# Performance work log

Measured on AMD Instinct MI355X. Metric: run time of the kernel, lower is better.

The kernel has to match this reference:

```python
import jax, jax.numpy as jnp
import numpy as np

B, T, D, H = 512, 256, 128, 512


def setup_inputs() -> dict:
    key = jax.random.key(0)
    ks = jax.random.split(key, 12)
    stdv_g = 1.0 / np.sqrt(D)            # gate layers: in_features = 2D + H
    gin = 2 * D + H
    stdv_gate = 1.0 / np.sqrt(gin)
    u = lambda k, shape, s: jax.random.uniform(k, shape, jnp.float32, -s, s)
    inp = {
        "x": jax.random.normal(ks[0], (B, T, D), jnp.float32),
        "x_last_obsv": jax.random.normal(ks[1], (B, T, D), jnp.float32),
        "mask": (jax.random.uniform(ks[2], (B, T, D)) < 0.7).astype(jnp.float32),
        "delta": jax.random.uniform(ks[3], (B, T, D)) * 5.0,
        "x_mean": jnp.zeros((1, 1, D), jnp.float32),
        "Wz": u(ks[4], (H, gin), stdv_gate), "bz": u(ks[5], (H,), stdv_gate),
        "Wr": u(ks[6], (H, gin), stdv_gate), "br": u(ks[7], (H,), stdv_gate),
        "Wn": u(ks[8], (H, gin), stdv_gate), "bn": u(ks[9], (H,), stdv_gate),
        "Wgx": u(ks[10], (D, D), stdv_g), "bgx": u(ks[11], (D,), stdv_g),
        "Wgh": u(jax.random.fold_in(key, 100), (H, D), stdv_g),
        "bgh": u(jax.random.fold_in(key, 101), (H,), stdv_g),
    }
    return inp


def reference(x, x_last_obsv, mask, delta, x_mean, Wz, bz, Wr, br, Wn, bn,
              Wgx, bgx, Wgh, bgh):
    D_ = x.shape[-1]
    xbar = x_mean.reshape(-1)                      # (D,)
    Wgx_diag = jnp.eye(D_, dtype=Wgx.dtype) * Wgx  # FilterLinear diagonal mask

    def step(h, inputs):
        xt, xl, mt, dt = inputs                    # each (B, D)
        # input decay (Eq. 3): gamma_x = exp(-relu(W_gx @ delta + b))
        gx = jnp.exp(-jnp.maximum(0.0, dt @ Wgx_diag.T + bgx))
        x_tilde = mt * xt + (1.0 - mt) * (gx * xl + (1.0 - gx) * xbar)
        # hidden decay: gamma_h = exp(-relu(W_gh @ delta + b))
        gh = jnp.exp(-jnp.maximum(0.0, dt @ Wgh.T + bgh))
        h = gh * h
        comb = jnp.concatenate([x_tilde, h, mt], axis=1)   # (B, 2D+H)
        z = jax.nn.sigmoid(comb @ Wz.T + bz)
        r = jax.nn.sigmoid(comb @ Wr.T + br)
        comb_r = jnp.concatenate([x_tilde, r * h, mt], axis=1)
        h_tilde = jnp.tanh(comb_r @ Wn.T + bn)
        h = (1.0 - z) * h + z * h_tilde
        return h, None

    h0 = jnp.zeros((x.shape[0], Wz.shape[0]), x.dtype)
    seq = (jnp.swapaxes(x, 0, 1), jnp.swapaxes(x_last_obsv, 0, 1),
           jnp.swapaxes(mask, 0, 1), jnp.swapaxes(delta, 0, 1))  # (T, B, D)
    h_final, _ = jax.lax.scan(step, h0, seq)
    return h_final
```

## Files before the change

### kernel.cpp

```cpp
#include <hip/hip_runtime.h>
#include <hip/hip_bf16.h>
#include <cstdint>

typedef short v8s __attribute__((ext_vector_type(8)));
typedef float f32x4 __attribute__((ext_vector_type(4)));
typedef float f4 __attribute__((ext_vector_type(4)));

#define BB 512
#define TT 256
#define DD 128
#define HH 512
#define GINW 768

static __device__ __forceinline__ unsigned short f2b(float f) {
  __hip_bfloat16 h = __float2bfloat16(f);
  return __builtin_bit_cast(unsigned short, h);
}
static __device__ __forceinline__ unsigned long long pk4(float a, float b, float c, float d) {
  return (unsigned long long)f2b(a) | ((unsigned long long)f2b(b) << 16)
       | ((unsigned long long)f2b(c) << 32) | ((unsigned long long)f2b(d) << 48);
}
static __device__ __forceinline__ float sigm(float v) { return 1.f / (1.f + __expf(-v)); }
static __device__ __forceinline__ float tanh_f(float v) { return 1.f - 2.f / (__expf(2.f * v) + 1.f); }

#define MFMA(A, B, C) __builtin_amdgcn_mfma_f32_16x16x32_bf16((A), (B), (C), 0, 0, 0)

static __device__ __forceinline__ void load_frags16T(const unsigned short* base, v8s fr[16]) {
#pragma unroll
  for (int ks = 0; ks < 16; ++ks) {
    asm volatile("global_load_dwordx4 %0, %1, off sc0 sc1"
                 : "=v"(fr[ks]) : "v"(base + ks * 1024));
  }
  asm volatile("s_waitcnt vmcnt(0)" ::: "memory");
  __builtin_amdgcn_sched_barrier(0);
}

__global__ __launch_bounds__(256, 1) void k_seq(
    const float* __restrict__ x, const float* __restrict__ xl,
    const float* __restrict__ mk, const float* __restrict__ de,
    const float* __restrict__ xmean,
    const float* __restrict__ Wz, const float* __restrict__ bz,
    const float* __restrict__ Wr, const float* __restrict__ br,
    const float* __restrict__ Wn, const float* __restrict__ bn,
    const float* __restrict__ Wgx, const float* __restrict__ bgx,
    const float* __restrict__ Wgh, const float* __restrict__ bgh,
    unsigned short* __restrict__ PBUF, unsigned short* __restrict__ HBUF,
    unsigned int* __restrict__ BAR, float* __restrict__ out)
{
  __shared__ unsigned short XA[2][32 * 264];
  __shared__ unsigned short DLs[2][32 * 136];
  __shared__ unsigned short sl[32 * 36];
  __shared__ float cw[128], cbx[128], cxm[128];

  const int bid = blockIdx.x;
  const int g = bid & 15, j = bid >> 4;
  const int tid = threadIdx.x, wave = tid >> 6, lane = tid & 63;
  const int q = lane >> 4, ln = lane & 15;
  const int mh = wave >> 1, nh = wave & 1;
  const int b0 = g * 32, c0 = j * 32;
  const int mrow = mh * 16 + q * 4;
  const int arow = mh * 16 + ln;
  const int ccol = c0 + nh * 16 + ln;

  if (tid < 128) { cw[tid] = Wgx[tid * DD + tid]; cbx[tid] = bgx[tid]; cxm[tid] = xmean[tid]; }

  const float bzv = bz[ccol], brv = br[ccol], bnv = bn[ccol], bgv = bgh[ccol];

  v8s zb[16], rb[16], nb[16];
  {
    const size_t wro = (size_t)ccol * GINW + 128;
#pragma unroll
    for (int ks = 0; ks < 16; ++ks) {
      const float* pz = Wz + wro + ks * 32 + q * 8;
      const float* pr = Wr + wro + ks * 32 + q * 8;
      const float* pn = Wn + wro + ks * 32 + q * 8;
      v8s vz, vr, vn;
#pragma unroll
      for (int e = 0; e < 8; ++e) {
        vz[e] = (short)f2b(pz[e]); vr[e] = (short)f2b(pr[e]); vn[e] = (short)f2b(pn[e]);
      }
      zb[ks] = vz; rb[ks] = vr; nb[ks] = vn;
    }
  }
  v8s xzb[8], xrb[8], xnb[8];
  {
    const size_t wro = (size_t)ccol * GINW;
#pragma unroll
    for (int ks = 0; ks < 8; ++ks) {
      const size_t o = wro + ((ks < 4) ? (size_t)(ks * 32 + q * 8) : (size_t)(512 + ks * 32 + q * 8));
      const float* pz = Wz + o; const float* pr = Wr + o; const float* pn = Wn + o;
      v8s vz, vr, vn;
#pragma unroll
      for (int e = 0; e < 8; ++e) {
        vz[e] = (short)f2b(pz[e]); vr[e] = (short)f2b(pr[e]); vn[e] = (short)f2b(pn[e]);
      }
      xzb[ks] = vz; xrb[ks] = vr; xnb[ks] = vn;
    }
  }
  v8s gb[4];
  {
    const size_t wro = (size_t)ccol * DD;
#pragma unroll
    for (int ks = 0; ks < 4; ++ks) {
      const float* pg = Wgh + wro + ks * 32 + q * 8;
      v8s vg;
#pragma unroll
      for (int e = 0; e < 8; ++e) vg[e] = (short)f2b(pg[e]);
      gb[ks] = vg;
    }
  }

  float h_own[4] = {0.f, 0.f, 0.f, 0.f};
  unsigned int ep = 0;
  unsigned short* pb = PBUF + (size_t)(g * 2) * 32 * HH;
  unsigned short* hb = HBUF + (size_t)(g * 2) * 32 * HH;
  unsigned int* flg = BAR + g * 512;
  unsigned int* myf = flg + j * 32;

  const int erow = tid >> 3, ed0 = (tid & 7) * 16;
  const size_t xrowb = (size_t)(b0 + erow) * TT * DD;

  auto stage = [&](int bp, int tx) {
    const size_t bt = xrowb + (size_t)tx * DD + ed0;
    const int tn = (tx + 1 < TT) ? (tx + 1) : (TT - 1);
    const size_t bn_ = xrowb + (size_t)tn * DD + ed0;
    const f4* px  = (const f4*)(x + bt);
    const f4* pxl = (const f4*)(xl + bt);
    const f4* pmk = (const f4*)(mk + bt);
    const f4* pdl = (const f4*)(de + bt);
    const f4* pdn = (const f4*)(de + bn_);
#pragma unroll
    for (int c = 0; c < 4; ++c) {
      const int d = ed0 + c * 4;
      f4 wv  = *(const f4*)&cw[d];
      f4 bv  = *(const f4*)&cbx[d];
      f4 xmv = *(const f4*)&cxm[d];
      f4 xv = px[c], xlv = pxl[c], mkv = pmk[c], dv = pdl[c], dnv = pdn[c];
      float xt[4];
#pragma unroll
      for (int e = 0; e < 4; ++e) {
        float gx = __expf(-fmaxf(0.f, dv[e] * wv[e] + bv[e]));
        float q1 = gx * (xlv[e] - xmv[e]) + xmv[e];
        xt[e] = q1 + mkv[e] * (xv[e] - q1);
      }
      *(unsigned long long*)&XA[bp][erow * 264 + d]       = pk4(xt[0], xt[1], xt[2], xt[3]);
      *(unsigned long long*)&XA[bp][erow * 264 + 128 + d] = pk4(mkv[0], mkv[1], mkv[2], mkv[3]);
      *(unsigned long long*)&DLs[bp][erow * 136 + d]      = pk4(dnv[0], dnv[1], dnv[2], dnv[3]);
    }
  };

  f32x4 azc, arc, anc, agc;
  auto xgemm = [&](int bp) {
    f32x4 z_ = {0.f,0.f,0.f,0.f}, r_ = {0.f,0.f,0.f,0.f};
    f32x4 n_ = {0.f,0.f,0.f,0.f}, g_ = {0.f,0.f,0.f,0.f};
#pragma unroll
    for (int ks = 0; ks < 8; ++ks) {
      v8s a = *(const v8s*)&XA[bp][arow * 264 + ks * 32 + q * 8];
      z_ = MFMA(a, xzb[ks], z_);
      r_ = MFMA(a, xrb[ks], r_);
      n_ = MFMA(a, xnb[ks], n_);
    }
#pragma unroll
    for (int ks = 0; ks < 4; ++ks) {
      v8s a = *(const v8s*)&DLs[bp][arow * 136 + ks * 32 + q * 8];
      g_ = MFMA(a, gb[ks], g_);
    }
    azc = z_; arc = r_; anc = n_; agc = g_;
  };

  auto export_sl = [&](unsigned short* dst) {
    const int h4 = tid & 1, row = (tid >> 1) & 31, qq = tid >> 6;
    unsigned long long v = *(unsigned long long*)&sl[row * 36 + qq * 8 + h4 * 4];
    __hip_atomic_store((unsigned long long*)(dst + (size_t)(j * 1024 + qq * 256 + row * 8 + h4 * 4)),
                       v, __ATOMIC_RELAXED, __HIP_MEMORY_SCOPE_AGENT);
  };
  auto poll = [&]() {
    if (lane < 16 && lane != j) {
      const unsigned int* fp = flg + lane * 32;
      while (__hip_atomic_load(fp, __ATOMIC_RELAXED, __HIP_MEMORY_SCOPE_AGENT) < ep)
        __builtin_amdgcn_s_sleep(1);
    }
    __builtin_amdgcn_sched_barrier(0);
  };

  __syncthreads();
  stage(0, 0);
  __syncthreads();
  xgemm(0);

  for (int t = 0; t < TT; ++t) {
    const int par = t & 1;
    if (t > 0) {
      v8s fr[16];
      load_frags16T(hb + (size_t)((t - 1) & 1) * 32 * HH + q * 256 + arow * 8, fr);
#pragma unroll
      for (int ks = 0; ks < 16; ++ks) {
        azc = MFMA(fr[ks], zb[ks], azc);
        arc = MFMA(fr[ks], rb[ks], arc);
      }
    }
    float zz[4];
#pragma unroll
    for (int rg = 0; rg < 4; ++rg) {
      float z = sigm(azc[rg] + bzv);
      float r = sigm(arc[rg] + brv);
      zz[rg] = z;
      sl[(mrow + rg) * 36 + nh * 16 + ln] = f2b(r * h_own[rg]);
    }
    if (t > 0) {
      __syncthreads();
      export_sl(pb + (size_t)par * 32 * HH);
      __syncthreads();
      ++ep;
      if (tid == 0)
        __hip_atomic_store(myf, ep, __ATOMIC_RELAXED, __HIP_MEMORY_SCOPE_AGENT);
    }
    if (t < TT - 1) stage(par ^ 1, t + 1);
    if (t > 0) {
      poll();
      v8s fr[16];
      load_frags16T(pb + (size_t)par * 32 * HH + q * 256 + arow * 8, fr);
#pragma unroll
      for (int ks = 0; ks < 16; ++ks) anc = MFMA(fr[ks], nb[ks], anc);
    }
    if (t == TT - 1) {
#pragma unroll
      for (int rg = 0; rg < 4; ++rg) {
        float n = tanh_f(anc[rg] + bnv);
        out[(size_t)(b0 + mrow + rg) * HH + ccol] = (1.f - zz[rg]) * h_own[rg] + zz[rg] * n;
      }
    } else {
#pragma unroll
      for (int rg = 0; rg < 4; ++rg) {
        float n = tanh_f(anc[rg] + bnv);
        float hn = (1.f - zz[rg]) * h_own[rg] + zz[rg] * n;
        float hd = __expf(-fmaxf(0.f, agc[rg] + bgv)) * hn;
        h_own[rg] = hd;
        sl[(mrow + rg) * 36 + nh * 16 + ln] = f2b(hd);
      }
      __syncthreads();
      export_sl(hb + (size_t)par * 32 * HH);
      __syncthreads();
      ++ep;
      if (tid == 0)
        __hip_atomic_store(myf, ep, __ATOMIC_RELAXED, __HIP_MEMORY_SCOPE_AGENT);
      xgemm(par ^ 1);
      poll();
    }
  }
}

extern "C" void kernel_launch(void* const* d_in, const int* in_sizes, int n_in,
                              void* d_out, int out_size, void* d_ws, size_t ws_size,
                              hipStream_t stream)
{
  const float* x   = (const float*)d_in[0];
  const float* xl  = (const float*)d_in[1];
  const float* mk  = (const float*)d_in[2];
  const float* de  = (const float*)d_in[3];
  const float* xm  = (const float*)d_in[4];
  const float* Wz  = (const float*)d_in[5];
  const float* bz  = (const float*)d_in[6];
  const float* Wr  = (const float*)d_in[7];
  const float* br  = (const float*)d_in[8];
  const float* Wn  = (const float*)d_in[9];
  const float* bn  = (const float*)d_in[10];
  const float* Wgx = (const float*)d_in[11];
  const float* bgx = (const float*)d_in[12];
  const float* Wgh = (const float*)d_in[13];
  const float* bgh = (const float*)d_in[14];
  float* out = (float*)d_out;

  char* p = (char*)d_ws;
  auto take = [&](size_t bytes) { char* r = p; p += (bytes + 255) & ~(size_t)255; return r; };
  unsigned short* PBUF = (unsigned short*)take((size_t)16 * 2 * 32 * HH * 2);
  unsigned short* HBUF = (unsigned short*)take((size_t)16 * 2 * 32 * HH * 2);
  unsigned int*   BARp = (unsigned int*)take(16 * 2048);

  hipMemsetAsync(BARp, 0, 16 * 2048, stream);

  k_seq<<<dim3(256), dim3(256), 0, stream>>>(
      x, xl, mk, de, xm, Wz, bz, Wr, br, Wn, bn,
      Wgx, bgx, Wgh, bgh, PBUF, HBUF, BARp, out);

  (void)in_sizes; (void)n_in; (void)out_size; (void)ws_size;
}
```

Before: 1.745 ms.

## Specialize waves: half poll peers while the other half stages next step

Waves 2-3 now stage the next timestep's inputs alone (stage128) while waves 0-1 poll the cross-block flags, coordinated through a shared-memory pdone counter instead of having all waves stage and then poll. The hidden-state export is made non-blocking and overlapped with the next-step x-GEMM, followed by an explicit vmcnt wait before the flag is published. The intent is to take input staging and the x-GEMM off the critical path of the inter-block synchronisation. In exchange, staging runs on half the threads, and the spin-wait on a workgroup-scope LDS variable adds ordering and visibility risk.

```diff
diff --git a/kernel.cpp b/kernel.cpp
--- a/kernel.cpp
+++ b/kernel.cpp
@@ -24,16 +24,6 @@
 static __device__ __forceinline__ float tanh_f(float v) { return 1.f - 2.f / (__expf(2.f * v) + 1.f); }
 
 #define MFMA(A, B, C) __builtin_amdgcn_mfma_f32_16x16x32_bf16((A), (B), (C), 0, 0, 0)
-
-static __device__ __forceinline__ void load_frags16T(const unsigned short* base, v8s fr[16]) {
-#pragma unroll
-  for (int ks = 0; ks < 16; ++ks) {
-    asm volatile("global_load_dwordx4 %0, %1, off sc0 sc1"
-                 : "=v"(fr[ks]) : "v"(base + ks * 1024));
-  }
-  asm volatile("s_waitcnt vmcnt(0)" ::: "memory");
-  __builtin_amdgcn_sched_barrier(0);
-}
 
 __global__ __launch_bounds__(256, 1) void k_seq(
     const float* __restrict__ x, const float* __restrict__ xl,
@@ -51,6 +41,7 @@
   __shared__ unsigned short DLs[2][32 * 136];
   __shared__ unsigned short sl[32 * 36];
   __shared__ float cw[128], cbx[128], cxm[128];
+  __shared__ unsigned int pdone;
 
   const int bid = blockIdx.x;
   const int g = bid & 15, j = bid >> 4;
@@ -63,6 +54,7 @@
   const int ccol = c0 + nh * 16 + ln;
 
   if (tid < 128) { cw[tid] = Wgx[tid * DD + tid]; cbx[tid] = bgx[tid]; cxm[tid] = xmean[tid]; }
+  if (tid == 0) pdone = 0;
 
   const float bzv = bz[ccol], brv = br[ccol], bnv = bn[ccol], bgv = bgh[ccol];
 
@@ -149,6 +141,38 @@
     }
   };
 
+  auto stage128 = [&](int bp, int tx) {
+    const int tp = tid - 128;
+    const int er = tp >> 2, e0 = (tp & 3) * 32;
+    const size_t rb_ = (size_t)(b0 + er) * TT * DD;
+    const size_t bt = rb_ + (size_t)tx * DD + e0;
+    const int tn = (tx + 1 < TT) ? (tx + 1) : (TT - 1);
+    const size_t bn_ = rb_ + (size_t)tn * DD + e0;
+    const f4* px  = (const f4*)(x + bt);
+    const f4* pxl = (const f4*)(xl + bt);
+    const f4* pmk = (const f4*)(mk + bt);
+    const f4* pdl = (const f4*)(de + bt);
+    const f4* pdn = (const f4*)(de + bn_);
+#pragma unroll
+    for (int c = 0; c < 8; ++c) {
+      const int d = e0 + c * 4;
+      f4 wv  = *(const f4*)&cw[d];
+      f4 bv  = *(const f4*)&cbx[d];
+      f4 xmv = *(const f4*)&cxm[d];
+      f4 xv = px[c], xlv = pxl[c], mkv = pmk[c], dv = pdl[c], dnv = pdn[c];
+      float xt[4];
+#pragma unroll
+      for (int e = 0; e < 4; ++e) {
+        float gx = __expf(-fmaxf(0.f, dv[e] * wv[e] + bv[e]));
+        float q1 = gx * (xlv[e] - xmv[e]) + xmv[e];
+        xt[e] = q1 + mkv[e] * (xv[e] - q1);
+      }
+      *(unsigned long long*)&XA[bp][er * 264 + d]       = pk4(xt[0], xt[1], xt[2], xt[3]);
+      *(unsigned long long*)&XA[bp][er * 264 + 128 + d] = pk4(mkv[0], mkv[1], mkv[2], mkv[3]);
+      *(unsigned long long*)&DLs[bp][er * 136 + d]      = pk4(dnv[0], dnv[1], dnv[2], dnv[3]);
+    }
+  };
+
   f32x4 azc, arc, anc, agc;
   auto xgemm = [&](int bp) {
     f32x4 z_ = {0.f,0.f,0.f,0.f}, r_ = {0.f,0.f,0.f,0.f};
@@ -168,11 +192,29 @@
     azc = z_; arc = r_; anc = n_; agc = g_;
   };
 
-  auto export_sl = [&](unsigned short* dst) {
+  auto load_frags16T = [&](const unsigned short* base, v8s fr[16]) {
+#pragma unroll
+    for (int ks = 0; ks < 16; ++ks)
+      asm volatile("global_load_dwordx4 %0, %1, off sc0 sc1"
+                   : "=v"(fr[ks]) : "v"(base + ks * 1024));
+    asm volatile("s_waitcnt vmcnt(0)" ::: "memory");
+    __builtin_amdgcn_sched_barrier(0);
+  };
+
+  auto export_sl_nd = [&](unsigned short* dst) {
     const int h4 = tid & 1, row = (tid >> 1) & 31, qq = tid >> 6;
     unsigned long long v = *(unsigned long long*)&sl[row * 36 + qq * 8 + h4 * 4];
-    __hip_atomic_store((unsigned long long*)(dst + (size_t)(j * 1024 + qq * 256 + row * 8 + h4 * 4)),
-                       v, __ATOMIC_RELAXED, __HIP_MEMORY_SCOPE_AGENT);
+    __hip_atomic_store(
+        (unsigned long long*)(dst + (size_t)(j * 1024 + qq * 256 + row * 8 + h4 * 4)),
+        v, __ATOMIC_RELAXED, __HIP_MEMORY_SCOPE_AGENT);
+  };
+  auto export_sl = [&](unsigned short* dst) {
+    export_sl_nd(dst);
+    asm volatile("s_waitcnt vmcnt(0)" ::: "memory");
+  };
+  auto put_flag = [&]() {
+    if (tid == 0)
+      __hip_atomic_store(myf, ep, __ATOMIC_RELAXED, __HIP_MEMORY_SCOPE_AGENT);
   };
   auto poll = [&]() {
     if (lane < 16 && lane != j) {
@@ -212,12 +254,17 @@
       export_sl(pb + (size_t)par * 32 * HH);
       __syncthreads();
       ++ep;
-      if (tid == 0)
-        __hip_atomic_store(myf, ep, __ATOMIC_RELAXED, __HIP_MEMORY_SCOPE_AGENT);
-    }
-    if (t < TT - 1) stage(par ^ 1, t + 1);
+      put_flag();
+    }
+    if (t > 0 && (wave < 2 || t == TT - 1)) poll();
+    if (wave == 0 && lane == 0)
+      __hip_atomic_store(&pdone, ep, __ATOMIC_RELAXED, __HIP_MEMORY_SCOPE_WORKGROUP);
+    if (t < TT - 1 && wave >= 2) {
+      stage128(par ^ 1, t + 1);
+      while (__hip_atomic_load(&pdone, __ATOMIC_RELAXED, __HIP_MEMORY_SCOPE_WORKGROUP) < ep) {}
+    }
+    __builtin_amdgcn_sched_barrier(0);
     if (t > 0) {
-      poll();
       v8s fr[16];
       load_frags16T(pb + (size_t)par * 32 * HH + q * 256 + arow * 8, fr);
 #pragma unroll
@@ -239,12 +286,12 @@
         sl[(mrow + rg) * 36 + nh * 16 + ln] = f2b(hd);
       }
       __syncthreads();
-      export_sl(hb + (size_t)par * 32 * HH);
+      export_sl_nd(hb + (size_t)par * 32 * HH);
+      xgemm(par ^ 1);
+      asm volatile("s_waitcnt vmcnt(0)" ::: "memory");
       __syncthreads();
       ++ep;
-      if (tid == 0)
-        __hip_atomic_store(myf, ep, __ATOMIC_RELAXED, __HIP_MEMORY_SCOPE_AGENT);
-      xgemm(par ^ 1);
+      put_flag();
       poll();
     }
   }
```

Result: slower. 2.534 ms (+45.2%).
